# Kernel tuning notes

Measured on AMD Instinct MI355X. Metric: run time of the kernel, lower is better.

## Reference

```python
import jax, jax.numpy as jnp
import numpy as np

QMAX = 7.0   # int4 symmetric, narrow range [-7, 7] per weight; acts use [-8, 7]
QMIN = -8.0

def _ste_quant(v, scale, qmin, qmax):
    """Symmetric per-tensor fake-quant with straight-through estimator."""
    s = jax.lax.stop_gradient(scale)
    q = jnp.clip(jnp.round(v / s), qmin, qmax) * s
    return v + jax.lax.stop_gradient(q - v)


def setup_inputs() -> dict:
    key = jax.random.key(0)
    k1, k2, k3 = jax.random.split(key, 3)
    d_model, vocab = 1024, 50257
    x = jax.random.normal(k1, (2, 1024, d_model), jnp.float32)
    W = jax.random.normal(k2, (vocab, d_model), jnp.float32) * 0.02
    b = jax.random.normal(k3, (vocab,), jnp.float32) * 0.01
    return {"x": x, "W": W, "b": b}


def reference(x, W, b):
    # Activation quant: 4-bit signed, per-tensor scale from max-abs stats
    sx = jnp.max(jnp.abs(x)) / QMAX
    xq = _ste_quant(x, sx, QMIN, QMAX)
    # Weight quant: 4-bit signed per-tensor
    sw = jnp.max(jnp.abs(W)) / QMAX
    wq = _ste_quant(W, sw, QMIN, QMAX)
    # Int32 bias: quantized at the accumulator scale sx*sw (range huge -> round only)
    sb = jax.lax.stop_gradient(sx * sw)
    bq = b + jax.lax.stop_gradient(jnp.round(b / sb) * sb - b)
    # Quantized GEMM with int32-style accumulation, expressed as dequantized matmul
    logits = jnp.einsum('bsd,vd->bsv', xq, wq) + bq  # [B, S, vocab]
    return jax.nn.log_softmax(logits, axis=-1)
```

## Files before the change

kernel.cpp:

```cpp
#include <hip/hip_runtime.h>
#include <hip/hip_bf16.h>

#define N_VOCAB 50257
#define NB      393
#define N_PAD   50304
#define D_K     1024
#define M_ROWS  2048
#define GEMM_BLOCKS (NB * 16)
#define PER_XCD     (GEMM_BLOCKS/8)

typedef __attribute__((ext_vector_type(4))) int i32x4;

__device__ inline void async_copy16(const void* g, void* l) {
  auto* gp = (const __attribute__((address_space(1))) unsigned int*)g;
  auto* lp = (__attribute__((address_space(3))) unsigned int*)l;
  __builtin_amdgcn_global_load_lds(gp, lp, 16, 0, 0);
}

__device__ inline signed char qint(float v, float s) {
  float q = fminf(fmaxf(rintf(v / s), -8.f), 7.f);
  return (signed char)(int)q;
}

__global__ void absmax2_kernel(const float4* __restrict__ x, int nx4,
                               const float4* __restrict__ Wp, int nw4,
                               unsigned* __restrict__ amax) {
  const bool isx = blockIdx.x < 512;
  const float4* p = isx ? x : Wp;
  const int n4 = isx ? nx4 : nw4;
  const int b0 = isx ? blockIdx.x : blockIdx.x - 512;
  const int nb = isx ? 512 : (gridDim.x - 512);
  float m = 0.f;
  for (int i = b0 * blockDim.x + threadIdx.x; i < n4; i += nb * blockDim.x) {
    float4 v = p[i];
    m = fmaxf(m, fmaxf(fmaxf(fabsf(v.x), fabsf(v.y)),
                       fmaxf(fabsf(v.z), fabsf(v.w))));
  }
#pragma unroll
  for (int off = 32; off; off >>= 1) m = fmaxf(m, __shfl_xor(m, off));
  __shared__ float red[4];
  int tid = threadIdx.x;
  if ((tid & 63) == 0) red[tid >> 6] = m;
  __syncthreads();
  if (tid == 0) {
    m = fmaxf(fmaxf(red[0], red[1]), fmaxf(red[2], red[3]));
    atomicMax(&amax[isx ? 0 : 1], __float_as_uint(m));
  }
}

__global__ void quant_kernel(const float4* __restrict__ x,
                             const float4* __restrict__ Wp,
                             const float* __restrict__ b,
                             char4* __restrict__ qx, char4* __restrict__ qw,
                             float* __restrict__ bq,
                             const unsigned* __restrict__ amax) {
  const int bid = blockIdx.x;
  const int tid = threadIdx.x;
  const int nw4 = (N_VOCAB * D_K) / 4;
  if (bid < 2048) {
    int i = bid * 256 + tid;
    float s = __uint_as_float(amax[0]) * (1.0f / 7.0f);
    float4 v = x[i];
    char4 q;
    q.x = qint(v.x, s); q.y = qint(v.y, s);
    q.z = qint(v.z, s); q.w = qint(v.w, s);
    qx[i] = q;
  } else if (bid < 2048 + 50304) {
    int i = (bid - 2048) * 256 + tid;
    char4 q = {0, 0, 0, 0};
    if (i < nw4) {
      float s = __uint_as_float(amax[1]) * (1.0f / 7.0f);
      float4 v = Wp[i];
      q.x = qint(v.x, s); q.y = qint(v.y, s);
      q.z = qint(v.z, s); q.w = qint(v.w, s);
    }
    qw[i] = q;
  } else {
    int i = (bid - (2048 + 50304)) * 256 + tid;
    if (i < N_PAD) {
      float v = 0.f;
      if (i < N_VOCAB) {
        float sb = (__uint_as_float(amax[0]) * (1.0f / 7.0f)) *
                   (__uint_as_float(amax[1]) * (1.0f / 7.0f));
        v = rintf(b[i] / sb) * sb;
      }
      bq[i] = v;
    }
  }
}

__global__ __launch_bounds__(256, 4) void gemm_kernel(
    const signed char* __restrict__ qx,
    const signed char* __restrict__ qw,
    const float* __restrict__ bq,
    const unsigned* __restrict__ amax,
    float* __restrict__ outp,
    float* __restrict__ pmax,
    float* __restrict__ psum)
{
  constexpr int BK = 64;
  __shared__ __align__(16) signed char sA[2][128 * BK];
  __shared__ __align__(16) signed char sB[2][128 * BK];
  __shared__ float redMax[128][2];
  __shared__ float redSum[128][2];

  const int tid = threadIdx.x;
  const int l = tid & 63;
  const int w = tid >> 6;
  const int wr = w >> 1, wc = w & 1;

  const int bid = blockIdx.x;
  const int vb = (bid & 7) * PER_XCD + (bid >> 3);
  const int nb = vb >> 4;
  const int m0 = (vb & 15) * 128;
  const int n0 = nb * 128;

  const float sx = __uint_as_float(amax[0]) * (1.0f / 7.0f);
  const float sw = __uint_as_float(amax[1]) * (1.0f / 7.0f);
  const float scale = sx * sw;

  i32x4 acc[4][4] = {};

  const int srow = (l >> 2);
  const int scol = ((l & 3) ^ ((l >> 3) & 3)) * 16;

  auto stage = [&](int buf, int k0) {
#pragma unroll
    for (int i = 0; i < 2; ++i) {
      int c = w * 2 + i;
      int row = c * 16 + srow;
      async_copy16(qx + (size_t)(m0 + row) * D_K + k0 + scol,
                   &sA[buf][c * 1024]);
      async_copy16(qw + (size_t)(n0 + row) * D_K + k0 + scol,
                   &sB[buf][c * 1024]);
    }
  };

  stage(0, 0);
  __syncthreads();

  int cur = 0;
  constexpr int NT = D_K / BK;
  for (int kt = 0; kt < NT; ++kt) {
    if (kt + 1 < NT) stage(cur ^ 1, (kt + 1) * BK);

    i32x4 af[4], bfr[4];
#pragma unroll
    for (int mi = 0; mi < 4; ++mi) {
      int row = wr * 64 + mi * 16 + (l & 15);
      int kb = ((l >> 4) ^ ((row >> 1) & 3)) * 16;
      af[mi] = *(const i32x4*)&sA[cur][row * BK + kb];
    }
#pragma unroll
    for (int ni = 0; ni < 4; ++ni) {
      int row = wc * 64 + ni * 16 + (l & 15);
      int kb = ((l >> 4) ^ ((row >> 1) & 3)) * 16;
      bfr[ni] = *(const i32x4*)&sB[cur][row * BK + kb];
    }
#pragma unroll
    for (int mi = 0; mi < 4; ++mi)
#pragma unroll
      for (int ni = 0; ni < 4; ++ni)
        acc[mi][ni] = __builtin_amdgcn_mfma_i32_16x16x64_i8(
            af[mi], bfr[ni], acc[mi][ni], 0, 0, 0);

    __syncthreads();
    cur ^= 1;
  }

  bool valid[4];
  float bb[4];
#pragma unroll
  for (int ni = 0; ni < 4; ++ni) {
    int col = n0 + wc * 64 + ni * 16 + (l & 15);
    valid[ni] = (col < N_VOCAB);
    bb[ni] = valid[ni] ? bq[col] : 0.f;
  }
  float lg[4][4][4];
#pragma unroll
  for (int mi = 0; mi < 4; ++mi)
#pragma unroll
    for (int ni = 0; ni < 4; ++ni)
#pragma unroll
      for (int r = 0; r < 4; ++r)
        lg[mi][ni][r] = (float)acc[mi][ni][r] * scale + bb[ni];

  float rmax[4][4];
#pragma unroll
  for (int mi = 0; mi < 4; ++mi)
#pragma unroll
    for (int r = 0; r < 4; ++r) {
      float mval = -3.4e38f;
#pragma unroll
      for (int ni = 0; ni < 4; ++ni)
        if (valid[ni]) mval = fmaxf(mval, lg[mi][ni][r]);
#pragma unroll
      for (int off = 1; off < 16; off <<= 1)
        mval = fmaxf(mval, __shfl_xor(mval, off));
      rmax[mi][r] = mval;
      if ((l & 15) == 0)
        redMax[wr * 64 + mi * 16 + (l >> 4) * 4 + r][wc] = mval;
    }
  __syncthreads();

#pragma unroll
  for (int mi = 0; mi < 4; ++mi)
#pragma unroll
    for (int r = 0; r < 4; ++r) {
      int rl = wr * 64 + mi * 16 + (l >> 4) * 4 + r;
      float gmax = fmaxf(redMax[rl][0], redMax[rl][1]);
      float s = 0.f;
#pragma unroll
      for (int ni = 0; ni < 4; ++ni)
        if (valid[ni]) s += __expf(lg[mi][ni][r] - gmax);
#pragma unroll
      for (int off = 1; off < 16; off <<= 1)
        s += __shfl_xor(s, off);
      if ((l & 15) == 0) redSum[rl][wc] = s;
      rmax[mi][r] = gmax;
    }
  __syncthreads();

  if (wc == 0 && (l & 15) == 0) {
#pragma unroll
    for (int mi = 0; mi < 4; ++mi)
#pragma unroll
      for (int r = 0; r < 4; ++r) {
        int rl = wr * 64 + mi * 16 + (l >> 4) * 4 + r;
        int rowg = m0 + rl;
        pmax[(size_t)rowg * NB + nb] = rmax[mi][r];
        psum[(size_t)rowg * NB + nb] = redSum[rl][0] + redSum[rl][1];
      }
  }

  float* wscr =
      reinterpret_cast<float*>((w < 2) ? &sA[0][0] : &sB[0][0]) +
      (w & 1) * 1100;
  const int q = l >> 4, j = l & 15;
  const int c0 = (4 - q) & 3;

#pragma unroll
  for (int mi = 0; mi < 4; ++mi) {
#pragma unroll
    for (int ni = 0; ni < 4; ++ni)
#pragma unroll
      for (int r = 0; r < 4; ++r)
        wscr[((l >> 4) * 4 + r) * 65 + ni * 16 + (l & 15)] = lg[mi][ni][r];
    asm volatile("" ::: "memory");
#pragma unroll
    for (int it = 0; it < 4; ++it) {
      int rl = it * 4 + q;
      int rowg = m0 + wr * 64 + mi * 16 + rl;
      size_t rbase = (size_t)rowg * N_VOCAB + n0 + wc * 64;
      if (j < 15) {
        int c = c0 + 4 * j;
        float4 v = *(const float4*)&wscr[rl * 65 + c];
        int colg = n0 + wc * 64 + c;
        if (colg + 3 < N_VOCAB) {
          *(float4*)&outp[rbase + c] = v;
        } else {
          const float* vv = (const float*)&v;
#pragma unroll
          for (int e = 0; e < 4; ++e)
            if (colg + e < N_VOCAB) outp[rbase + c + e] = vv[e];
        }
      } else if (c0 == 0) {
        int c = 60;
        float4 v = *(const float4*)&wscr[rl * 65 + c];
        int colg = n0 + wc * 64 + c;
        if (colg + 3 < N_VOCAB) {
          *(float4*)&outp[rbase + c] = v;
        } else {
          const float* vv = (const float*)&v;
#pragma unroll
          for (int e = 0; e < 4; ++e)
            if (colg + e < N_VOCAB) outp[rbase + c + e] = vv[e];
        }
      } else {
        for (int c = 0; c < c0; ++c) {
          int colg = n0 + wc * 64 + c;
          if (colg < N_VOCAB) outp[rbase + c] = wscr[rl * 65 + c];
        }
        for (int c = c0 + 60; c < 64; ++c) {
          int colg = n0 + wc * 64 + c;
          if (colg < N_VOCAB) outp[rbase + c] = wscr[rl * 65 + c];
        }
      }
    }
    asm volatile("" ::: "memory");
  }
}

__global__ __launch_bounds__(256) void finalize_kernel(
    const float* __restrict__ pmax, const float* __restrict__ psum,
    float* __restrict__ logz) {
  const int row = blockIdx.x;
  const float* pm = pmax + (size_t)row * NB;
  const float* ps = psum + (size_t)row * NB;
  const int tid = threadIdx.x;
  __shared__ float red[8];

  float m = -3.4e38f;
  for (int i = tid; i < NB; i += 256) m = fmaxf(m, pm[i]);
#pragma unroll
  for (int off = 32; off; off >>= 1) m = fmaxf(m, __shfl_xor(m, off));
  if ((tid & 63) == 0) red[tid >> 6] = m;
  __syncthreads();
  m = fmaxf(fmaxf(red[0], red[1]), fmaxf(red[2], red[3]));

  float s = 0.f;
  for (int i = tid; i < NB; i += 256) s += ps[i] * __expf(pm[i] - m);
#pragma unroll
  for (int off = 32; off; off >>= 1) s += __shfl_xor(s, off);
  if ((tid & 63) == 0) red[4 + (tid >> 6)] = s;
  __syncthreads();
  if (tid == 0) {
    s = red[4] + red[5] + red[6] + red[7];
    logz[row] = m + __logf(s);
  }
}

__global__ __launch_bounds__(256) void subtract_kernel(
    float* __restrict__ out, const float* __restrict__ logz) {
  const int row = blockIdx.x;
  const float lz = logz[row];
  const size_t base = (size_t)row * N_VOCAB;
  const int tid = threadIdx.x;
  const int a = (4 - (row & 3)) & 3;
  if (tid < a) out[base + tid] -= lz;
  const int n4 = (N_VOCAB - a) >> 2;
  float4* p = (float4*)(out + base + a);
  for (int i = tid; i < n4; i += 256) {
    float4 v = p[i];
    v.x -= lz; v.y -= lz; v.z -= lz; v.w -= lz;
    p[i] = v;
  }
  const int done = a + n4 * 4;
  if (tid < N_VOCAB - done) out[base + done + tid] -= lz;
}

extern "C" void kernel_launch(void* const* d_in, const int* in_sizes, int n_in,
                              void* d_out, int out_size, void* d_ws,
                              size_t ws_size, hipStream_t stream) {
  const float* x = (const float*)d_in[0];
  const float* W = (const float*)d_in[1];
  const float* b = (const float*)d_in[2];
  float* out = (float*)d_out;

  char* ws = (char*)d_ws;
  unsigned* amax = (unsigned*)ws;
  float* bq = (float*)(ws + 4096);
  float* logz = (float*)(ws + (1ull << 20));
  float* pmax = (float*)(ws + (2ull << 20));
  float* psum = (float*)(ws + (6ull << 20));
  signed char* qx = (signed char*)(ws + (10ull << 20));
  signed char* qw = (signed char*)(ws + (14ull << 20));

  hipMemsetAsync(amax, 0, 8, stream);

  const int nx4 = (M_ROWS * D_K) / 4;
  const int nw4 = (N_VOCAB * D_K) / 4;

  absmax2_kernel<<<2560, 256, 0, stream>>>((const float4*)x, nx4,
                                           (const float4*)W, nw4, amax);

  quant_kernel<<<2048 + 50304 + 197, 256, 0, stream>>>(
      (const float4*)x, (const float4*)W, b, (char4*)qx, (char4*)qw, bq, amax);

  gemm_kernel<<<GEMM_BLOCKS, 256, 0, stream>>>(qx, qw, bq, amax, out, pmax,
                                               psum);

  finalize_kernel<<<M_ROWS, 256, 0, stream>>>(pmax, psum, logz);

  subtract_kernel<<<M_ROWS, 256, 0, stream>>>(out, logz);
}
```

Baseline: 608.8 us.

## Triple-buffer GEMM K-loop with finer waits and write logits directly

Moves the int8 GEMM main loop from a double buffer to a triple buffer with prefetch distance two. The __syncthreads is replaced by explicit vmcnt waits, raw barriers and s_setprio around the MFMAs, aiming to hide global-to-LDS load latency and cut barrier stalls. The LDS-staged, float4-vectorized epilogue store is replaced by direct per-lane scalar stores of the logits. The extra LDS buffer lowers occupancy from 4 to 3 blocks, and the scalar stores are less coalesced, so the output write, which is a large share of the time, may get slower.

Measured after the change: 577.4 us. -5.2%, faster.

```diff
diff --git a/kernel.cpp b/kernel.cpp
--- a/kernel.cpp
+++ b/kernel.cpp
@@ -89,7 +89,7 @@
   }
 }
 
-__global__ __launch_bounds__(256, 4) void gemm_kernel(
+__global__ __launch_bounds__(256, 3) void gemm_kernel(
     const signed char* __restrict__ qx,
     const signed char* __restrict__ qw,
     const float* __restrict__ bq,
@@ -99,8 +99,9 @@
     float* __restrict__ psum)
 {
   constexpr int BK = 64;
-  __shared__ __align__(16) signed char sA[2][128 * BK];
-  __shared__ __align__(16) signed char sB[2][128 * BK];
+  constexpr int NT = D_K / BK;
+  __shared__ __align__(16) signed char sA[3][128 * BK];
+  __shared__ __align__(16) signed char sB[3][128 * BK];
   __shared__ float redMax[128][2];
   __shared__ float redSum[128][2];
 
@@ -124,7 +125,8 @@
   const int srow = (l >> 2);
   const int scol = ((l & 3) ^ ((l >> 3) & 3)) * 16;
 
-  auto stage = [&](int buf, int k0) {
+  auto stage = [&](int buf, int kt) {
+    int k0 = kt * BK;
 #pragma unroll
     for (int i = 0; i < 2; ++i) {
       int c = w * 2 + i;
@@ -137,12 +139,14 @@
   };
 
   stage(0, 0);
-  __syncthreads();
-
-  int cur = 0;
-  constexpr int NT = D_K / BK;
+  stage(1, 1);
+  asm volatile("s_waitcnt vmcnt(4)" ::: "memory");
+  __builtin_amdgcn_s_barrier();
+  __builtin_amdgcn_sched_barrier(0);
+
+#pragma unroll
   for (int kt = 0; kt < NT; ++kt) {
-    if (kt + 1 < NT) stage(cur ^ 1, (kt + 1) * BK);
+    const int cur = kt % 3;
 
     i32x4 af[4], bfr[4];
 #pragma unroll
@@ -157,15 +161,27 @@
       int kb = ((l >> 4) ^ ((row >> 1) & 3)) * 16;
       bfr[ni] = *(const i32x4*)&sB[cur][row * BK + kb];
     }
+
+    if (kt + 2 < NT) stage((kt + 2) % 3, kt + 2);
+
+    __builtin_amdgcn_s_setprio(1);
 #pragma unroll
     for (int mi = 0; mi < 4; ++mi)
 #pragma unroll
       for (int ni = 0; ni < 4; ++ni)
         acc[mi][ni] = __builtin_amdgcn_mfma_i32_16x16x64_i8(
             af[mi], bfr[ni], acc[mi][ni], 0, 0, 0);
-
-    __syncthreads();
-    cur ^= 1;
+    __builtin_amdgcn_s_setprio(0);
+    __builtin_amdgcn_sched_barrier(0);
+
+    if (kt + 1 < NT) {
+      if (kt + 2 < NT)
+        asm volatile("s_waitcnt vmcnt(4)" ::: "memory");
+      else
+        asm volatile("s_waitcnt vmcnt(0)" ::: "memory");
+      __builtin_amdgcn_s_barrier();
+      __builtin_amdgcn_sched_barrier(0);
+    }
   }
 
   bool valid[4];
@@ -233,62 +249,20 @@
       }
   }
 
-  float* wscr =
-      reinterpret_cast<float*>((w < 2) ? &sA[0][0] : &sB[0][0]) +
-      (w & 1) * 1100;
-  const int q = l >> 4, j = l & 15;
-  const int c0 = (4 - q) & 3;
-
-#pragma unroll
-  for (int mi = 0; mi < 4; ++mi) {
-#pragma unroll
-    for (int ni = 0; ni < 4; ++ni)
-#pragma unroll
-      for (int r = 0; r < 4; ++r)
-        wscr[((l >> 4) * 4 + r) * 65 + ni * 16 + (l & 15)] = lg[mi][ni][r];
-    asm volatile("" ::: "memory");
-#pragma unroll
-    for (int it = 0; it < 4; ++it) {
-      int rl = it * 4 + q;
-      int rowg = m0 + wr * 64 + mi * 16 + rl;
-      size_t rbase = (size_t)rowg * N_VOCAB + n0 + wc * 64;
-      if (j < 15) {
-        int c = c0 + 4 * j;
-        float4 v = *(const float4*)&wscr[rl * 65 + c];
-        int colg = n0 + wc * 64 + c;
-        if (colg + 3 < N_VOCAB) {
-          *(float4*)&outp[rbase + c] = v;
-        } else {
-          const float* vv = (const float*)&v;
-#pragma unroll
-          for (int e = 0; e < 4; ++e)
-            if (colg + e < N_VOCAB) outp[rbase + c + e] = vv[e];
-        }
-      } else if (c0 == 0) {
-        int c = 60;
-        float4 v = *(const float4*)&wscr[rl * 65 + c];
-        int colg = n0 + wc * 64 + c;
-        if (colg + 3 < N_VOCAB) {
-          *(float4*)&outp[rbase + c] = v;
-        } else {
-          const float* vv = (const float*)&v;
-#pragma unroll
-          for (int e = 0; e < 4; ++e)
-            if (colg + e < N_VOCAB) outp[rbase + c + e] = vv[e];
-        }
-      } else {
-        for (int c = 0; c < c0; ++c) {
-          int colg = n0 + wc * 64 + c;
-          if (colg < N_VOCAB) outp[rbase + c] = wscr[rl * 65 + c];
-        }
-        for (int c = c0 + 60; c < 64; ++c) {
-          int colg = n0 + wc * 64 + c;
-          if (colg < N_VOCAB) outp[rbase + c] = wscr[rl * 65 + c];
+#pragma unroll
+  for (int mi = 0; mi < 4; ++mi)
+#pragma unroll
+    for (int r = 0; r < 4; ++r) {
+      int rowg = m0 + wr * 64 + mi * 16 + (l >> 4) * 4 + r;
+      size_t rb = (size_t)rowg * N_VOCAB;
+#pragma unroll
+      for (int ni = 0; ni < 4; ++ni) {
+        if (valid[ni]) {
+          int col = n0 + wc * 64 + ni * 16 + (l & 15);
+          outp[rb + col] = lg[mi][ni][r];
         }
       }
     }
-    asm volatile("" ::: "memory");
-  }
 }
 
 __global__ __launch_bounds__(256) void finalize_kernel(
```
